# Optimization experiments

Hardware: AMD Instinct MI355X
Metric: run time of the kernel (lower is better)

Reference implementation:

```python
import jax, jax.numpy as jnp
import numpy as np

N_QUBITS = 6      # 4 data + 2 ancilla
N_DATA = 4
N_LAYERS = 4
N_GROUPS = 8
DIM = 2 ** N_QUBITS  # 64 statevector amplitudes (real: RY + CNOT keep state real)
GN_GROUPS = 32
EPS = 1e-5


def _cnot_ring_perm():
    # CNOT(q, q+1 mod n) ring applied sequentially; compose into one basis permutation.
    n = N_QUBITS
    f = np.arange(DIM)
    for c in range(n):
        t = (c + 1) % n
        cbit = (f >> (n - 1 - c)) & 1
        f = np.where(cbit == 1, f ^ (1 << (n - 1 - t)), f)
    # new_state[f[i]] = old_state[i]  =>  new = old[finv]
    finv = np.empty(DIM, dtype=np.int64)
    finv[f] = np.arange(DIM)
    return jnp.asarray(finv)


def _zsign():
    i = np.arange(DIM)[:, None]
    q = np.arange(N_DATA)[None, :]
    return jnp.asarray(1.0 - 2.0 * ((i >> (N_QUBITS - 1 - q)) & 1), dtype=jnp.float32)


PERM = _cnot_ring_perm()
ZSIGN = _zsign()


def _group_norm(x, gamma, beta):
    B, C, H, W = x.shape
    xg = x.reshape(B, GN_GROUPS, C // GN_GROUPS, H, W)
    mu = xg.mean(axis=(2, 3, 4), keepdims=True)
    var = xg.var(axis=(2, 3, 4), keepdims=True)
    xn = ((xg - mu) * jax.lax.rsqrt(var + EPS)).reshape(B, C, H, W)
    return xn * gamma[None, :, None, None] + beta[None, :, None, None]


def _apply_ry(state, half_angle, q):
    # state: [B,H,W,G,64]; half_angle: [B,H,W,G]; RY = [[c,-s],[s,c]] on qubit q
    pre, post = 2 ** q, 2 ** (N_QUBITS - 1 - q)
    s = state.reshape(state.shape[:-1] + (pre, 2, post))
    c = jnp.cos(half_angle)[..., None, None]
    sn = jnp.sin(half_angle)[..., None, None]
    a0, a1 = s[..., 0, :], s[..., 1, :]
    new = jnp.stack([c * a0 - sn * a1, sn * a0 + c * a1], axis=-2)
    return new.reshape(state.shape)


def _forward(x, emb, gamma, beta, w_in, b_in, theta, w_style, b_style, w_out, b_out):
    B, C, H, W = x.shape
    h = _group_norm(x, gamma, beta)                       # norm0
    emb_a = emb * jax.nn.sigmoid(emb)                     # SiLU(emb)
    # 1x1 projection to per-group data-qubit rotation angles: [B,H,W,G,4]
    ang = jnp.einsum('oc,bchw->bohw', w_in, h) + b_in[None, :, None, None]
    ang = ang.reshape(B, N_GROUPS, N_DATA, H, W).transpose(0, 3, 4, 1, 2)
    # style modulation of circuit parameters: [B,G,L,Q]
    style = (emb_a @ w_style.T + b_style).reshape(B, N_GROUPS, N_LAYERS, N_QUBITS)
    # init |0...0> per pixel per group
    state = jnp.zeros((B, H, W, N_GROUPS, DIM), x.dtype).at[..., 0].set(1.0)
    for l in range(N_LAYERS):
        for q in range(N_QUBITS):
            a = theta[:, l, q][None, None, None, :] + style[:, :, l, q][:, None, None, :]
            if q < N_DATA:                                # data reuploading each layer
                a = a + ang[..., q]
            state = _apply_ry(state, 0.5 * a, q)
        state = state[..., PERM]                          # CNOT ring entangler
    probs = state * state
    meas = probs @ ZSIGN                                  # [B,H,W,G,4] <Z> on data qubits
    meas = meas.transpose(0, 3, 4, 1, 2).reshape(B, N_GROUPS * N_DATA, H, W)
    out = jnp.einsum('oc,bchw->bohw', w_out, meas) + b_out[None, :, None, None]
    return out + x                                        # residual


def setup_inputs() -> dict:
    key = jax.random.key(0)
    ks = jax.random.split(key, 6)
    B, C, H, W, E = 16, 256, 32, 32, 512
    return {
        'x': jax.random.normal(ks[0], (B, C, H, W), jnp.float32),
        'emb': jax.random.normal(ks[1], (B, E), jnp.float32),
        'gamma': jnp.ones((C,), jnp.float32),
        'beta': jnp.zeros((C,), jnp.float32),
        'w_in': jax.random.normal(ks[2], (32, C), jnp.float32) * 0.1,
        'b_in': jnp.zeros((32,), jnp.float32),
        'theta': jax.random.normal(ks[3], (N_GROUPS, N_LAYERS, N_QUBITS), jnp.float32) * 0.5,
        'w_style': jax.random.normal(ks[4], (N_GROUPS * N_LAYERS * N_QUBITS, E), jnp.float32) * 0.02,
        'b_style': jnp.zeros((N_GROUPS * N_LAYERS * N_QUBITS,), jnp.float32),
        'w_out': jax.random.normal(ks[5], (C, 32), jnp.float32) * 0.05,
        'b_out': jnp.zeros((C,), jnp.float32),
    }


def reference(x, emb, gamma, beta, w_in, b_in, theta, w_style, b_style, w_out, b_out):
    return _forward(x, emb, gamma, beta, w_in, b_in, theta, w_style, b_style, w_out, b_out)
```

## Files before the change

### kernel.cpp

```cpp
#include <hip/hip_runtime.h>
#include <math.h>

#define NB 16
#define NC 256
#define NHW 1024
#define NE 512
#define NDQ 4
#define NLQ 4
#define NQB 6
#define QDIM 64
#define PIX 16
#define XPAD 260

typedef float v2f __attribute__((ext_vector_type(2)));

constexpr int fwd1(int i) {
    int r = i;
    for (int c = 0; c < NQB; ++c) {
        int t = (c + 1) % NQB;
        if ((r >> (NQB - 1 - c)) & 1) r ^= 1 << (NQB - 1 - t);
    }
    return r;
}
constexpr int fwdl(int s, int l) { for (int i = 0; i < l; ++i) s = fwd1(s); return s; }
constexpr int parity6(int x) { x ^= x >> 4; x ^= x >> 2; x ^= x >> 1; return x & 1; }

struct GateTab { int M[NLQ][NQB]; int V[NLQ][NQB]; int W[NDQ]; };
constexpr GateTab make_tab() {
    GateTab g{};
    for (int l = 0; l < NLQ; ++l)
        for (int q = 0; q < NQB; ++q) {
            int m = 1 << (NQB - 1 - q);
            for (int x = 0; x < QDIM; ++x) if (fwdl(x, l) == m) { g.M[l][q] = x; break; }
            int V = 0;
            for (int t = 0; t < NQB; ++t) V |= ((fwdl(1 << t, l) >> (NQB - 1 - q)) & 1) << t;
            g.V[l][q] = V;
        }
    for (int d = 0; d < NDQ; ++d) {
        int W = 0;
        for (int t = 0; t < NQB; ++t) W |= ((fwdl(1 << t, NLQ) >> (NQB - 1 - d)) & 1) << t;
        g.W[d] = W;
    }
    return g;
}
constexpr GateTab GT = make_tab();

__global__ __launch_bounds__(256) void k_pre(const float* __restrict__ x,
                                             const float* __restrict__ emb,
                                             const float* __restrict__ w_style,
                                             const float* __restrict__ b_style,
                                             const float* __restrict__ theta,
                                             float* __restrict__ mu,
                                             float* __restrict__ rs,
                                             float* __restrict__ A) {
    if (blockIdx.x < 512) {
        int bg = blockIdx.x;
        const float4* xp = (const float4*)(x + (size_t)bg * 8 * NHW);
        float s = 0.f, ss = 0.f;
        for (int i = threadIdx.x; i < 8 * NHW / 4; i += 256) {
            float4 v = xp[i];
            s  += v.x + v.y + v.z + v.w;
            ss += v.x*v.x + v.y*v.y + v.z*v.z + v.w*v.w;
        }
        __shared__ float red0[4], red1[4];
        #pragma unroll
        for (int o = 32; o; o >>= 1) { s += __shfl_down(s, o); ss += __shfl_down(ss, o); }
        int lane = threadIdx.x & 63, w = threadIdx.x >> 6;
        if (lane == 0) { red0[w] = s; red1[w] = ss; }
        __syncthreads();
        if (threadIdx.x == 0) {
            s  = red0[0] + red0[1] + red0[2] + red0[3];
            ss = red1[0] + red1[1] + red1[2] + red1[3];
            float m = s * (1.f / 8192.f);
            float var = ss * (1.f / 8192.f) - m * m;
            mu[bg] = m;
            rs[bg] = rsqrtf(var + 1e-5f);
        }
    } else {
        int b = blockIdx.x - 512;
        __shared__ float es[NE];
        int t = threadIdx.x;
        for (int i = t; i < NE; i += 256) {
            float v = emb[b * NE + i];
            es[i] = v / (1.f + __expf(-v));
        }
        __syncthreads();
        int j0 = t >> 3, sub = t & 7;
        for (int pass = 0; pass < 6; ++pass) {
            int j = pass * 32 + j0;
            const float* wr = w_style + (size_t)j * NE + sub * 64;
            const float* er = es + sub * 64;
            float acc = 0.f;
            #pragma unroll
            for (int i = 0; i < 64; i += 4) {
                float4 w4 = *(const float4*)(wr + i);
                acc = fmaf(w4.x, er[i],   acc);
                acc = fmaf(w4.y, er[i+1], acc);
                acc = fmaf(w4.z, er[i+2], acc);
                acc = fmaf(w4.w, er[i+3], acc);
            }
            acc += __shfl_xor(acc, 1);
            acc += __shfl_xor(acc, 2);
            acc += __shfl_xor(acc, 4);
            if (sub == 0) A[b * 192 + j] = theta[j] + b_style[j] + acc;
        }
    }
}

__global__ __launch_bounds__(256, 2) void k_main(
    const float* __restrict__ x,
    const float* __restrict__ gamma,
    const float* __restrict__ beta,
    const float* __restrict__ w_in,
    const float* __restrict__ b_in,
    const float* __restrict__ A,
    const float* __restrict__ w_out,
    const float* __restrict__ b_out,
    const float* __restrict__ mu,
    const float* __restrict__ rs,
    float* __restrict__ out) {

    __shared__ float xs[PIX * XPAD];
    __shared__ float as_[PIX * 36];

    int blk = blockIdx.x;
    int b = blk >> 6;
    int pbase = (blk & 63) * PIX;
    int t = threadIdx.x;
    int c0 = t >> 2, f4 = (t & 3) * 4;

    float4 xr[4];
    #pragma unroll
    for (int k = 0; k < 4; ++k) {
        int c = c0 + 64 * k;
        xr[k] = *(const float4*)(x + (size_t)(b * NC + c) * NHW + pbase + f4);
    }

    #pragma unroll
    for (int k = 0; k < 4; ++k) {
        int c = c0 + 64 * k;
        int g = b * 32 + (c >> 3);
        float sc = rs[g] * gamma[c];
        float sh = fmaf(-mu[g], sc, beta[c]);
        float4 v = xr[k];
        float* bp = xs + f4 * XPAD + c;
        bp[0]        = fmaf(v.x, sc, sh);
        bp[XPAD]     = fmaf(v.y, sc, sh);
        bp[2 * XPAD] = fmaf(v.z, sc, sh);
        bp[3 * XPAD] = fmaf(v.w, sc, sh);
    }
    __syncthreads();

    {
        int og = t >> 4, p = t & 15;
        int o0 = og * 2;
        const float* hrow = xs + p * XPAD;
        const float* w0r = w_in + o0 * NC;
        const float* w1r = w_in + (o0 + 1) * NC;
        v2f a0 = {0.f, 0.f}, a1 = {0.f, 0.f};
        #pragma unroll 8
        for (int c = 0; c < NC; c += 4) {
            float4 h = *(const float4*)(hrow + c);
            v2f hlo = {h.x, h.y}, hhi = {h.z, h.w};
            float4 w0 = *(const float4*)(w0r + c);
            float4 w1 = *(const float4*)(w1r + c);
            a0 = __builtin_elementwise_fma((v2f){w0.x, w0.y}, hlo, a0);
            a0 = __builtin_elementwise_fma((v2f){w0.z, w0.w}, hhi, a0);
            a1 = __builtin_elementwise_fma((v2f){w1.x, w1.y}, hlo, a1);
            a1 = __builtin_elementwise_fma((v2f){w1.z, w1.w}, hhi, a1);
        }
        as_[p * 36 + o0]     = a0.x + a0.y + b_in[o0];
        as_[p * 36 + o0 + 1] = a1.x + a1.y + b_in[o0 + 1];
    }
    __syncthreads();

    #pragma unroll
    for (int k = 0; k < 4; ++k) {
        int c = c0 + 64 * k;
        float4 v = xr[k];
        float* bp = xs + f4 * XPAD + c;
        bp[0] = v.x; bp[XPAD] = v.y; bp[2 * XPAD] = v.z; bp[3 * XPAD] = v.w;
    }

    if (t < 128) {
        int g = t >> 4, p = t & 15;
        float4 angv = *(const float4*)(as_ + p * 36 + g * 4);
        float angp[NDQ] = {angv.x, angv.y, angv.z, angv.w};
        float Ar[24];
        {
            const float4* Ab4 = (const float4*)(A + b * 192 + g * 24);
            #pragma unroll
            for (int j = 0; j < 6; ++j) {
                float4 a4 = Ab4[j];
                Ar[4*j] = a4.x; Ar[4*j+1] = a4.y; Ar[4*j+2] = a4.z; Ar[4*j+3] = a4.w;
            }
        }

        v2f st2[32];
        #pragma unroll
        for (int k = 0; k < 32; ++k) st2[k] = (v2f){0.f, 0.f};
        st2[0].x = 1.f;

        #pragma unroll
        for (int l = 0; l < NLQ; ++l) {
            #pragma unroll
            for (int q = 0; q < NQB; ++q) {
                const int M = GT.M[l][q], V = GT.V[l][q];
                const int KD = M >> 1, SW = M & 1;
                int hh = KD; hh |= hh >> 1; hh |= hh >> 2; hh |= hh >> 4;
                const int HB = hh - (hh >> 1);
                float a = Ar[l * NQB + q] + (q < NDQ ? angp[q] : 0.f);
                float sn, cs;
                __sincosf(0.5f * a, &sn, &cs);
                v2f cs2 = {cs, cs};
                v2f sPP = {sn, sn}, sPM = {sn, -sn}, sMP = {-sn, sn}, sMM = {-sn, -sn};
                auto COV = [&](int i0) -> v2f {
                    bool p0 = parity6(i0 & V), p1 = parity6((i0 + 1) & V);
                    return p0 ? (p1 ? sPP : sPM) : (p1 ? sMP : sMM);
                };
                if (KD == 0) {
                    #pragma unroll
                    for (int k = 0; k < 32; ++k) {
                        v2f ov = __builtin_shufflevector(st2[k], st2[k], 1, 0);
                        st2[k] = __builtin_elementwise_fma(COV(2*k), ov, cs2 * st2[k]);
                    }
                } else {
                    #pragma unroll
                    for (int k = 0; k < 32; ++k) {
                        if (k & HB) continue;
                        int kp = k ^ KD;
                        v2f av = st2[k], bv = st2[kp];
                        v2f am = SW ? __builtin_shufflevector(av, av, 1, 0) : av;
                        v2f bm = SW ? __builtin_shufflevector(bv, bv, 1, 0) : bv;
                        st2[k]  = __builtin_elementwise_fma(COV(2*k),  bm, cs2 * av);
                        st2[kp] = __builtin_elementwise_fma(COV(2*kp), am, cs2 * bv);
                    }
                }
            }
        }

        #pragma unroll
        for (int k = 0; k < 32; ++k) st2[k] = st2[k] * st2[k];
        float md[NDQ];
        #pragma unroll
        for (int d = 0; d < NDQ; ++d) {
            const int W = GT.W[d];
            v2f acc = {0.f, 0.f};
            #pragma unroll
            for (int k = 0; k < 32; ++k) {
                v2f sg = { parity6((2*k)     & W) ? -1.f : 1.f,
                           parity6((2*k + 1) & W) ? -1.f : 1.f };
                acc = __builtin_elementwise_fma(sg, st2[k], acc);
            }
            md[d] = acc.x + acc.y;
        }
        float4 mv = {md[0], md[1], md[2], md[3]};
        *(float4*)(as_ + p * 36 + g * 4) = mv;
    }
    __syncthreads();

    {
        int c2 = t >> 3, f2 = (t & 7) * 2;
        v2f mreg[32];
        #pragma unroll
        for (int j = 0; j < 8; ++j) {
            float4 ma = *(const float4*)(as_ + (f2 + 0) * 36 + 4 * j);
            float4 mb = *(const float4*)(as_ + (f2 + 1) * 36 + 4 * j);
            mreg[4*j + 0] = (v2f){ma.x, mb.x};
            mreg[4*j + 1] = (v2f){ma.y, mb.y};
            mreg[4*j + 2] = (v2f){ma.z, mb.z};
            mreg[4*j + 3] = (v2f){ma.w, mb.w};
        }
        #pragma unroll
        for (int k = 0; k < 8; ++k) {
            int c = c2 + 32 * k;
            const float* wr = w_out + c * 32;
            v2f acc = {0.f, 0.f};
            #pragma unroll
            for (int j = 0; j < 8; ++j) {
                float4 w = *(const float4*)(wr + 4 * j);
                acc = __builtin_elementwise_fma((v2f){w.x, w.x}, mreg[4*j + 0], acc);
                acc = __builtin_elementwise_fma((v2f){w.y, w.y}, mreg[4*j + 1], acc);
                acc = __builtin_elementwise_fma((v2f){w.z, w.z}, mreg[4*j + 2], acc);
                acc = __builtin_elementwise_fma((v2f){w.w, w.w}, mreg[4*j + 3], acc);
            }
            float bo = b_out[c];
            float x0 = xs[(f2 + 0) * XPAD + c];
            float x1 = xs[(f2 + 1) * XPAD + c];
            float2 r = {acc.x + bo + x0, acc.y + bo + x1};
            *(float2*)(out + (size_t)(b * NC + c) * NHW + pbase + f2) = r;
        }
    }
}

extern "C" void kernel_launch(void* const* d_in, const int* in_sizes, int n_in,
                              void* d_out, int out_size, void* d_ws, size_t ws_size,
                              hipStream_t stream) {
    const float* x       = (const float*)d_in[0];
    const float* emb     = (const float*)d_in[1];
    const float* gamma   = (const float*)d_in[2];
    const float* beta    = (const float*)d_in[3];
    const float* w_in    = (const float*)d_in[4];
    const float* b_in    = (const float*)d_in[5];
    const float* theta   = (const float*)d_in[6];
    const float* w_style = (const float*)d_in[7];
    const float* b_style = (const float*)d_in[8];
    const float* w_out   = (const float*)d_in[9];
    const float* b_out   = (const float*)d_in[10];
    float* out = (float*)d_out;

    float* ws = (float*)d_ws;
    float* mu = ws;
    float* rs = ws + 512;
    float* A  = ws + 1024;

    k_pre<<<512 + NB, 256, 0, stream>>>(x, emb, w_style, b_style, theta, mu, rs, A);
    k_main<<<NB * 64, 256, 0, stream>>>(x, gamma, beta, w_in, b_in, A,
                                        w_out, b_out, mu, rs, out);
}
```

Before: 138.8 us.

## Use bf16 MFMA for input and output 1x1 projections

```diff
diff --git a/kernel.cpp b/kernel.cpp
--- a/kernel.cpp
+++ b/kernel.cpp
@@ -10,9 +10,17 @@
 #define NQB 6
 #define QDIM 64
 #define PIX 16
-#define XPAD 260
+#define HSS 264
 
 typedef float v2f __attribute__((ext_vector_type(2)));
+typedef float f32x4 __attribute__((ext_vector_type(4)));
+typedef short bf16x8 __attribute__((ext_vector_type(8)));
+
+__device__ __forceinline__ short f2bf(float v) {
+    unsigned u = __builtin_bit_cast(unsigned, v);
+    u += 0x7FFFu + ((u >> 16) & 1u);
+    return (short)(u >> 16);
+}
 
 constexpr int fwd1(int i) {
     int r = i;
@@ -50,9 +58,12 @@
                                              const float* __restrict__ w_style,
                                              const float* __restrict__ b_style,
                                              const float* __restrict__ theta,
+                                             const float* __restrict__ w_in,
+                                             const float* __restrict__ w_out,
                                              float* __restrict__ mu,
                                              float* __restrict__ rs,
-                                             float* __restrict__ A) {
+                                             float* __restrict__ A,
+                                             short* __restrict__ wbf) {
     if (blockIdx.x < 512) {
         int bg = blockIdx.x;
         const float4* xp = (const float4*)(x + (size_t)bg * 8 * NHW);
@@ -76,7 +87,7 @@
             mu[bg] = m;
             rs[bg] = rsqrtf(var + 1e-5f);
         }
-    } else {
+    } else if (blockIdx.x < 512 + NB) {
         int b = blockIdx.x - 512;
         __shared__ float es[NE];
         int t = threadIdx.x;
@@ -104,6 +115,9 @@
             acc += __shfl_xor(acc, 4);
             if (sub == 0) A[b * 192 + j] = theta[j] + b_style[j] + acc;
         }
+    } else {
+        for (int i = threadIdx.x; i < 8192; i += 256) wbf[i] = f2bf(w_in[i]);
+        for (int i = threadIdx.x; i < 8192; i += 256) wbf[8192 + i] = f2bf(w_out[i]);
     }
 }
 
@@ -111,29 +125,41 @@
     const float* __restrict__ x,
     const float* __restrict__ gamma,
     const float* __restrict__ beta,
-    const float* __restrict__ w_in,
     const float* __restrict__ b_in,
     const float* __restrict__ A,
-    const float* __restrict__ w_out,
+    const short* __restrict__ w_in_bf,
+    const short* __restrict__ w_out_bf,
     const float* __restrict__ b_out,
     const float* __restrict__ mu,
     const float* __restrict__ rs,
     float* __restrict__ out) {
 
-    __shared__ float xs[PIX * XPAD];
+    __shared__ short hs[PIX * HSS];
+    __shared__ float xs2[NC * PIX];
     __shared__ float as_[PIX * 36];
 
     int blk = blockIdx.x;
     int b = blk >> 6;
     int pbase = (blk & 63) * PIX;
     int t = threadIdx.x;
+    int lane = t & 63, wv = t >> 6;
     int c0 = t >> 2, f4 = (t & 3) * 4;
+    int nn = lane & 15, quad = lane >> 4;
 
     float4 xr[4];
     #pragma unroll
     for (int k = 0; k < 4; ++k) {
         int c = c0 + 64 * k;
         xr[k] = *(const float4*)(x + (size_t)(b * NC + c) * NHW + pbase + f4);
+        *(float4*)(xs2 + c * PIX + f4) = xr[k];
+    }
+
+    bf16x8 bfrag[8];
+    if (wv >= 2) {
+        int o = ((wv - 2) << 4) + nn;
+        #pragma unroll
+        for (int s = 0; s < 8; ++s)
+            bfrag[s] = *(const bf16x8*)(w_in_bf + o * NC + s * 32 + quad * 8);
     }
 
     #pragma unroll
@@ -143,44 +169,27 @@
         float sc = rs[g] * gamma[c];
         float sh = fmaf(-mu[g], sc, beta[c]);
         float4 v = xr[k];
-        float* bp = xs + f4 * XPAD + c;
-        bp[0]        = fmaf(v.x, sc, sh);
-        bp[XPAD]     = fmaf(v.y, sc, sh);
-        bp[2 * XPAD] = fmaf(v.z, sc, sh);
-        bp[3 * XPAD] = fmaf(v.w, sc, sh);
+        hs[(f4 + 0) * HSS + c] = f2bf(fmaf(v.x, sc, sh));
+        hs[(f4 + 1) * HSS + c] = f2bf(fmaf(v.y, sc, sh));
+        hs[(f4 + 2) * HSS + c] = f2bf(fmaf(v.z, sc, sh));
+        hs[(f4 + 3) * HSS + c] = f2bf(fmaf(v.w, sc, sh));
     }
     __syncthreads();
 
-    {
-        int og = t >> 4, p = t & 15;
-        int o0 = og * 2;
-        const float* hrow = xs + p * XPAD;
-        const float* w0r = w_in + o0 * NC;
-        const float* w1r = w_in + (o0 + 1) * NC;
-        v2f a0 = {0.f, 0.f}, a1 = {0.f, 0.f};
-        #pragma unroll 8
-        for (int c = 0; c < NC; c += 4) {
-            float4 h = *(const float4*)(hrow + c);
-            v2f hlo = {h.x, h.y}, hhi = {h.z, h.w};
-            float4 w0 = *(const float4*)(w0r + c);
-            float4 w1 = *(const float4*)(w1r + c);
-            a0 = __builtin_elementwise_fma((v2f){w0.x, w0.y}, hlo, a0);
-            a0 = __builtin_elementwise_fma((v2f){w0.z, w0.w}, hhi, a0);
-            a1 = __builtin_elementwise_fma((v2f){w1.x, w1.y}, hlo, a1);
-            a1 = __builtin_elementwise_fma((v2f){w1.z, w1.w}, hhi, a1);
-        }
-        as_[p * 36 + o0]     = a0.x + a0.y + b_in[o0];
-        as_[p * 36 + o0 + 1] = a1.x + a1.y + b_in[o0 + 1];
+    if (wv >= 2) {
+        f32x4 acc = {0.f, 0.f, 0.f, 0.f};
+        #pragma unroll
+        for (int s = 0; s < 8; ++s) {
+            bf16x8 afr = *(const bf16x8*)(hs + nn * HSS + s * 32 + quad * 8);
+            acc = __builtin_amdgcn_mfma_f32_16x16x32_bf16(afr, bfrag[s], acc, 0, 0, 0);
+        }
+        int o = ((wv - 2) << 4) + nn;
+        float bi = b_in[o];
+        #pragma unroll
+        for (int r = 0; r < 4; ++r)
+            as_[(quad * 4 + r) * 36 + o] = acc[r] + bi;
     }
     __syncthreads();
-
-    #pragma unroll
-    for (int k = 0; k < 4; ++k) {
-        int c = c0 + 64 * k;
-        float4 v = xr[k];
-        float* bp = xs + f4 * XPAD + c;
-        bp[0] = v.x; bp[XPAD] = v.y; bp[2 * XPAD] = v.z; bp[3 * XPAD] = v.w;
-    }
 
     if (t < 128) {
         int g = t >> 4, p = t & 15;
@@ -260,35 +269,25 @@
     __syncthreads();
 
     {
-        int c2 = t >> 3, f2 = (t & 7) * 2;
-        v2f mreg[32];
-        #pragma unroll
-        for (int j = 0; j < 8; ++j) {
-            float4 ma = *(const float4*)(as_ + (f2 + 0) * 36 + 4 * j);
-            float4 mb = *(const float4*)(as_ + (f2 + 1) * 36 + 4 * j);
-            mreg[4*j + 0] = (v2f){ma.x, mb.x};
-            mreg[4*j + 1] = (v2f){ma.y, mb.y};
-            mreg[4*j + 2] = (v2f){ma.z, mb.z};
-            mreg[4*j + 3] = (v2f){ma.w, mb.w};
-        }
-        #pragma unroll
-        for (int k = 0; k < 8; ++k) {
-            int c = c2 + 32 * k;
-            const float* wr = w_out + c * 32;
-            v2f acc = {0.f, 0.f};
-            #pragma unroll
-            for (int j = 0; j < 8; ++j) {
-                float4 w = *(const float4*)(wr + 4 * j);
-                acc = __builtin_elementwise_fma((v2f){w.x, w.x}, mreg[4*j + 0], acc);
-                acc = __builtin_elementwise_fma((v2f){w.y, w.y}, mreg[4*j + 1], acc);
-                acc = __builtin_elementwise_fma((v2f){w.z, w.z}, mreg[4*j + 2], acc);
-                acc = __builtin_elementwise_fma((v2f){w.w, w.w}, mreg[4*j + 3], acc);
-            }
+        float4 m0 = *(const float4*)(as_ + nn * 36 + quad * 8);
+        float4 m1 = *(const float4*)(as_ + nn * 36 + quad * 8 + 4);
+        bf16x8 afr = { f2bf(m0.x), f2bf(m0.y), f2bf(m0.z), f2bf(m0.w),
+                       f2bf(m1.x), f2bf(m1.y), f2bf(m1.z), f2bf(m1.w) };
+        #pragma unroll
+        for (int ti = 0; ti < 4; ++ti) {
+            int tile = wv * 4 + ti;
+            int c = tile * 16 + nn;
+            bf16x8 bfr = *(const bf16x8*)(w_out_bf + c * 32 + quad * 8);
+            f32x4 acc = {0.f, 0.f, 0.f, 0.f};
+            acc = __builtin_amdgcn_mfma_f32_16x16x32_bf16(afr, bfr, acc, 0, 0, 0);
             float bo = b_out[c];
-            float x0 = xs[(f2 + 0) * XPAD + c];
-            float x1 = xs[(f2 + 1) * XPAD + c];
-            float2 r = {acc.x + bo + x0, acc.y + bo + x1};
-            *(float2*)(out + (size_t)(b * NC + c) * NHW + pbase + f2) = r;
+            float4 x4 = *(const float4*)(xs2 + c * PIX + quad * 4);
+            float4 r;
+            r.x = acc[0] + bo + x4.x;
+            r.y = acc[1] + bo + x4.y;
+            r.z = acc[2] + bo + x4.z;
+            r.w = acc[3] + bo + x4.w;
+            *(float4*)(out + (size_t)(b * NC + c) * NHW + pbase + quad * 4) = r;
         }
     }
 }
@@ -313,8 +312,10 @@
     float* mu = ws;
     float* rs = ws + 512;
     float* A  = ws + 1024;
-
-    k_pre<<<512 + NB, 256, 0, stream>>>(x, emb, w_style, b_style, theta, mu, rs, A);
-    k_main<<<NB * 64, 256, 0, stream>>>(x, gamma, beta, w_in, b_in, A,
-                                        w_out, b_out, mu, rs, out);
-}
+    short* wbf = (short*)(ws + 4096);
+
+    k_pre<<<512 + NB + 1, 256, 0, stream>>>(x, emb, w_style, b_style, theta,
+                                            w_in, w_out, mu, rs, A, wbf);
+    k_main<<<NB * 64, 256, 0, stream>>>(x, gamma, beta, b_in, A,
+                                        wbf, wbf + 8192, b_out, mu, rs, out);
+}
```

Result: faster. 120.4 us (-13.3%).
